# Kernel optimization log

Hardware: AMD Instinct MI355X
Metric: run time of the kernel (lower is better)

## Reference

```python
import jax, jax.numpy as jnp
import numpy as np

HW = 16          # feature map side before crop
P = HW * HW      # 256 spatial positions
G = 128          # output genetic channels per branch
CROP = 14        # crop size


def feature_genetic(x, idx, oh, ow):
    # x: [B, C, 16, 16]; idx: [G, P] channel index per (group, position);
    # oh, ow: [G] crop offsets in {0,1}
    B = x.shape[0]
    feat = x.reshape(B, x.shape[1], P)                 # [B, C, 256]
    pos = jnp.arange(P)
    picked = feat[:, idx, pos]                         # [B, G, 256]
    grid = picked.reshape(B, G, HW, HW)                # [B, 128, 16, 16]
    ch = jnp.arange(G)
    hidx = oh[:, None] + jnp.arange(CROP)[None, :]     # [G, 14]
    widx = ow[:, None] + jnp.arange(CROP)[None, :]     # [G, 14]
    # fancy-index crop: [B, 128, 14, 14]
    return grid[:, ch[:, None, None], hidx[:, :, None], widx[:, None, :]]


def setup_inputs() -> dict:
    key = jax.random.key(0)
    k1, k3, k5, kw, ki, kh, kw2 = jax.random.split(key, 7)
    B, C = 128, 512
    x1 = jax.random.normal(k1, (B, C, HW, HW), dtype=jnp.float32)
    x3 = jax.random.normal(k3, (B, C, HW, HW), dtype=jnp.float32)
    x5 = jax.random.normal(k5, (B, C, HW, HW), dtype=jnp.float32)
    W = jax.random.normal(kw, (768, 384), dtype=jnp.float32) * 0.02  # 1x1 conv weight
    idx = jax.random.randint(ki, (3, G, P), 0, C, dtype=jnp.int32)
    offh = jax.random.randint(kh, (3, G), 0, 2, dtype=jnp.int32)
    offw = jax.random.randint(kw2, (3, G), 0, 2, dtype=jnp.int32)
    return {"x1": x1, "x3": x3, "x5": x5, "W": W, "idx": idx, "offh": offh, "offw": offw}


def reference(x1, x3, x5, W, idx, offh, offw):
    g1 = feature_genetic(x1, idx[0], offh[0], offw[0])   # [B, 128, 14, 14]
    g3 = feature_genetic(x3, idx[1], offh[1], offw[1])
    g5 = feature_genetic(x5, idx[2], offh[2], offw[2])
    feats = jnp.concatenate((g1, g3, g5), axis=1)        # [B, 384, 14, 14]
    # 1x1 conv (no bias): Conv2d(384, 768, kernel_size=1)
    out = jnp.einsum('bchw,oc->bohw', feats, W)          # [B, 768, 14, 14]
    return out
```

## Files before the change

### kernel.cpp

```cpp
#include <hip/hip_runtime.h>
#include <hip/hip_bf16.h>

#define PIX 256
#define CROP 14
#define HW2 196
#define BB 128
#define CC 512
#define NC 384
#define NO 768
#define CAP 128

typedef __bf16 bf16x8 __attribute__((ext_vector_type(8)));
typedef __bf16 bf16x4 __attribute__((ext_vector_type(4)));
typedef float  f32x4  __attribute__((ext_vector_type(4)));
typedef unsigned int u32;

#define GLOAD_LDS16(src, dst) \
    __builtin_amdgcn_global_load_lds((const __attribute__((address_space(1))) void*)(src), \
                                     (__attribute__((address_space(3))) void*)(dst), 16, 0, 0)

__global__ void wconv_kernel(const float* __restrict__ W, __bf16* __restrict__ Wb) {
    int tid = blockIdx.x * 256 + threadIdx.x;
    Wb[tid] = (__bf16)W[tid];
}

__global__ void fill_kernel(const int* __restrict__ idx, const int* __restrict__ offh,
                            const int* __restrict__ offw, int* __restrict__ cnt,
                            u32* __restrict__ bucket) {
    int tid = blockIdx.x * 256 + threadIdx.x;
    int c3 = tid / HW2;
    int hw = tid - c3 * HW2;
    int i = hw / CROP, j = hw - i * CROP;
    int p = (offh[c3] + i) * 16 + offw[c3] + j;
    int ch = idx[c3 * PIX + p];
    int bkt = (c3 >> 7) * CC + ch;
    int pos = atomicAdd(&cnt[bkt], 1);
    if (pos < CAP) bucket[bkt * CAP + pos] = ((u32)c3 << 16) | ((u32)hw << 8) | (u32)p;
}

#define LSTR 260
__global__ __launch_bounds__(256) void scatter_kernel(
        const float* __restrict__ x1, const float* __restrict__ x3,
        const float* __restrict__ x5, const int* __restrict__ cnt,
        const u32* __restrict__ bucket, __bf16* __restrict__ fT) {
    __shared__ __bf16 lds[64 * LSTR];
    int bx = blockIdx.x;
    int E = cnt[bx]; if (E > CAP) E = CAP;
    if (E == 0) return;
    int b0 = blockIdx.y * 64;
    int t = bx >> 9, ch = bx & 511;
    const float* x = (t == 0) ? x1 : (t == 1) ? x3 : x5;
    int w = threadIdx.x >> 6, lane = threadIdx.x & 63;
    for (int r = w; r < 64; r += 4) {
        f32x4 v = *(const f32x4*)(x + ((size_t)(b0 + r) * CC + ch) * PIX + lane * 4);
        bf16x4 q;
        q[0] = (__bf16)v[0]; q[1] = (__bf16)v[1]; q[2] = (__bf16)v[2]; q[3] = (__bf16)v[3];
        *(bf16x4*)&lds[r * LSTR + lane * 4] = q;
    }
    __syncthreads();
    for (int e = w; e < E; e += 4) {
        u32 pk = bucket[bx * CAP + e];
        int c3 = pk >> 16, hw = (pk >> 8) & 255, p = pk & 255;
        fT[((size_t)c3 * HW2 + hw) * BB + b0 + lane] = lds[lane * LSTR + p];
    }
}

__global__ __launch_bounds__(256) void ftrans_kernel(const __bf16* __restrict__ fT,
                                                     __bf16* __restrict__ feats) {
    __shared__ __bf16 lds[64 * 128];
    int hw = blockIdx.x;
    int c0 = blockIdx.y * 64;
    int t = threadIdx.x;
    int l16 = t & 15;
#pragma unroll
    for (int r4 = 0; r4 < 4; ++r4) {
        int cr = (t >> 4) + r4 * 16;
        bf16x8 v = *(const bf16x8*)(fT + ((size_t)(c0 + cr) * HW2 + hw) * BB + l16 * 8);
        int chunk = l16 ^ ((cr >> 3) & 7);
        *(bf16x8*)&lds[cr * 128 + chunk * 8] = v;
    }
    __syncthreads();
    int cg = t & 7;
#pragma unroll
    for (int r = 0; r < 4; ++r) {
        int b = (t >> 3) + r * 32;
        bf16x8 ov;
#pragma unroll
        for (int k = 0; k < 8; ++k) {
            int c = cg * 8 + k;
            ov[k] = lds[c * 128 + (((b >> 3) ^ cg) * 8) + (b & 7)];
        }
        *(bf16x8*)(feats + ((size_t)b * HW2 + hw) * NC + c0 + cg * 8) = ov;
    }
}

__global__ __launch_bounds__(256) void gemm_kernel(const __bf16* __restrict__ feats,
                                                   const __bf16* __restrict__ Wb,
                                                   float* __restrict__ out) {
    __shared__ __bf16 ldsbuf[16384];
    __bf16* Abuf = ldsbuf;
    __bf16* Bbuf = ldsbuf + 8192;

    const int d = blockIdx.x;
    const int wg = (d & 7) * 147 + (d >> 3);
    const int o_base = (wg % 6) * 128;
    const int m_base = (wg / 6) * 128;

    const int tid = threadIdx.x;
    const int wave = tid >> 6, lane = tid & 63;
    const int wo = wave >> 1, wm = wave & 1;
    const int l15 = lane & 15, g = lane >> 4;
    const int xr = l15 & 7;

    f32x4 acc[4][4] = {};

    for (int kt = 0; kt < 6; ++kt) {
        const int k0g = kt * 64;
#pragma unroll
        for (int it = 0; it < 4; ++it) {
            int ck = tid + it * 256;
            int row = ck >> 3, cc = ck & 7;
            int koff = k0g + ((cc ^ (row & 7)) << 3);
            GLOAD_LDS16(Wb    + (size_t)(o_base + row) * NC + koff, Abuf + ck * 8);
            GLOAD_LDS16(feats + (size_t)(m_base + row) * NC + koff, Bbuf + ck * 8);
        }
        __syncthreads();
#pragma unroll
        for (int k0 = 0; k0 < 64; k0 += 32) {
            const int cb = (k0 >> 3) + g;
            bf16x8 a[4], b[4];
#pragma unroll
            for (int s = 0; s < 4; ++s) {
                int arow = wo * 64 + s * 16 + l15;
                a[s] = *(const bf16x8*)&Abuf[arow * 64 + ((cb ^ xr) << 3)];
                int brow = wm * 64 + s * 16 + l15;
                b[s] = *(const bf16x8*)&Bbuf[brow * 64 + ((cb ^ xr) << 3)];
            }
#pragma unroll
            for (int os = 0; os < 4; ++os)
#pragma unroll
                for (int ms = 0; ms < 4; ++ms)
                    acc[os][ms] = __builtin_amdgcn_mfma_f32_16x16x32_bf16(a[os], b[ms], acc[os][ms], 0, 0, 0);
        }
        __syncthreads();
    }

#pragma unroll
    for (int os = 0; os < 4; ++os)
#pragma unroll
        for (int ms = 0; ms < 4; ++ms) {
            int m = m_base + wm * 64 + ms * 16 + l15;
            int bb = m / HW2;
            int hw = m - bb * HW2;
            int o = o_base + wo * 64 + os * 16 + g * 4;
            float* dst = out + ((size_t)bb * NO + o) * HW2 + hw;
            f32x4 v = acc[os][ms];
            dst[0 * HW2] = v[0];
            dst[1 * HW2] = v[1];
            dst[2 * HW2] = v[2];
            dst[3 * HW2] = v[3];
        }
}

extern "C" void kernel_launch(void* const* d_in, const int* in_sizes, int n_in,
                              void* d_out, int out_size, void* d_ws, size_t ws_size,
                              hipStream_t stream) {
    const float* x1   = (const float*)d_in[0];
    const float* x3   = (const float*)d_in[1];
    const float* x5   = (const float*)d_in[2];
    const float* W    = (const float*)d_in[3];
    const int*   idx  = (const int*)d_in[4];
    const int*   offh = (const int*)d_in[5];
    const int*   offw = (const int*)d_in[6];
    float* out = (float*)d_out;

    char* ws = (char*)d_ws;
    __bf16* fT     = (__bf16*)(ws);
    __bf16* feats  = (__bf16*)(ws + 19267584);
    __bf16* Wb     = (__bf16*)(ws + 38535168);
    int*    cnt    = (int*)   (ws + 39124992);
    u32*    bucket = (u32*)   (ws + 39131136);

    wconv_kernel<<<(NO * NC) / 256, 256, 0, stream>>>(W, Wb);
    hipMemsetAsync(cnt, 0, 1536 * sizeof(int), stream);
    fill_kernel<<<(NC * HW2) / 256, 256, 0, stream>>>(idx, offh, offw, cnt, bucket);
    scatter_kernel<<<dim3(1536, 2), 256, 0, stream>>>(x1, x3, x5, cnt, bucket, fT);
    ftrans_kernel<<<dim3(HW2, 6), 256, 0, stream>>>(fT, feats);
    gemm_kernel<<<1176, 256, 0, stream>>>(feats, Wb, out);
}
```

Measured before the change: 110.3 us.

## Replace bucketed scatter plus transpose with per-batch gather into LDS

The per-channel bucket scatter, which wrote a channel-major intermediate, and the separate transpose kernel are replaced by a prefix scan and compaction of the bucket entries into one dense list per branch. A new per-(batch, branch) kernel gathers the selected elements directly from x into an LDS tile and writes feats rows coalesced. This removes the fT intermediate round trip and the transpose pass, but the gathers from x are now scattered 4-byte loads rather than whole-row vector loads. It also adds two small launches, one of them a single-block scan.

```diff
diff --git a/kernel.cpp b/kernel.cpp
--- a/kernel.cpp
+++ b/kernel.cpp
@@ -9,6 +9,7 @@
 #define NC 384
 #define NO 768
 #define CAP 128
+#define ENT_T 25088
 
 typedef __bf16 bf16x8 __attribute__((ext_vector_type(8)));
 typedef __bf16 bf16x4 __attribute__((ext_vector_type(4)));
@@ -35,62 +36,81 @@
     int ch = idx[c3 * PIX + p];
     int bkt = (c3 >> 7) * CC + ch;
     int pos = atomicAdd(&cnt[bkt], 1);
-    if (pos < CAP) bucket[bkt * CAP + pos] = ((u32)c3 << 16) | ((u32)hw << 8) | (u32)p;
-}
-
-#define LSTR 260
+    if (pos < CAP)
+        bucket[bkt * CAP + pos] =
+            ((u32)(c3 & 127) << 25) | ((u32)hw << 17) | ((u32)p << 9) | (u32)ch;
+}
+
+__global__ __launch_bounds__(256) void scan_kernel(const int* __restrict__ cnt,
+                                                   int* __restrict__ pref) {
+    __shared__ int part[256];
+    int tid = threadIdx.x;
+    int loc[6];
+    int s = 0;
+#pragma unroll
+    for (int i = 0; i < 6; ++i) {
+        int v = cnt[tid * 6 + i]; if (v > CAP) v = CAP;
+        loc[i] = s; s += v;
+    }
+    part[tid] = s;
+    __syncthreads();
+    if (tid < 64) {
+        int l4[4]; int s4 = 0;
+#pragma unroll
+        for (int i = 0; i < 4; ++i) { l4[i] = s4; s4 += part[tid * 4 + i]; }
+        int v = s4;
+#pragma unroll
+        for (int d = 1; d < 64; d <<= 1) { int u = __shfl_up(v, d); if (tid >= d) v += u; }
+        int excl = v - s4;
+#pragma unroll
+        for (int i = 0; i < 4; ++i) part[tid * 4 + i] = excl + l4[i];
+    }
+    __syncthreads();
+    int off = part[tid];
+#pragma unroll
+    for (int i = 0; i < 6; ++i) pref[tid * 6 + i] = off + loc[i];
+}
+
+__global__ __launch_bounds__(128) void compact_kernel(const int* __restrict__ cnt,
+                                                      const int* __restrict__ pref,
+                                                      const u32* __restrict__ bucket,
+                                                      u32* __restrict__ ent) {
+    int bkt = blockIdx.x;
+    int E = cnt[bkt]; if (E > CAP) E = CAP;
+    int tid = threadIdx.x;
+    if (tid < E) ent[pref[bkt] + tid] = bucket[bkt * CAP + tid];
+}
+
 __global__ __launch_bounds__(256) void scatter_kernel(
         const float* __restrict__ x1, const float* __restrict__ x3,
-        const float* __restrict__ x5, const int* __restrict__ cnt,
-        const u32* __restrict__ bucket, __bf16* __restrict__ fT) {
-    __shared__ __bf16 lds[64 * LSTR];
-    int bx = blockIdx.x;
-    int E = cnt[bx]; if (E > CAP) E = CAP;
-    if (E == 0) return;
-    int b0 = blockIdx.y * 64;
-    int t = bx >> 9, ch = bx & 511;
+        const float* __restrict__ x5, const u32* __restrict__ ent,
+        __bf16* __restrict__ feats) {
+    __shared__ __bf16 fl[HW2 * 128];
+    int blk = blockIdx.x;
+    int b = blk / 3;
+    int t = blk - b * 3;
     const float* x = (t == 0) ? x1 : (t == 1) ? x3 : x5;
-    int w = threadIdx.x >> 6, lane = threadIdx.x & 63;
-    for (int r = w; r < 64; r += 4) {
-        f32x4 v = *(const f32x4*)(x + ((size_t)(b0 + r) * CC + ch) * PIX + lane * 4);
-        bf16x4 q;
-        q[0] = (__bf16)v[0]; q[1] = (__bf16)v[1]; q[2] = (__bf16)v[2]; q[3] = (__bf16)v[3];
-        *(bf16x4*)&lds[r * LSTR + lane * 4] = q;
+    const float* xb = x + (size_t)b * CC * PIX;
+    const u32* el = ent + t * ENT_T;
+    int tid = threadIdx.x;
+
+#pragma unroll 4
+    for (int g = tid; g < ENT_T; g += 256) {
+        u32 wd = el[g];
+        int ch = wd & 511;
+        int p  = (wd >> 9) & 255;
+        int hw = (wd >> 17) & 255;
+        int c3 = wd >> 25;
+        float f = xb[ch * PIX + p];
+        fl[hw * 128 + c3] = (__bf16)f;
     }
     __syncthreads();
-    for (int e = w; e < E; e += 4) {
-        u32 pk = bucket[bx * CAP + e];
-        int c3 = pk >> 16, hw = (pk >> 8) & 255, p = pk & 255;
-        fT[((size_t)c3 * HW2 + hw) * BB + b0 + lane] = lds[lane * LSTR + p];
-    }
-}
-
-__global__ __launch_bounds__(256) void ftrans_kernel(const __bf16* __restrict__ fT,
-                                                     __bf16* __restrict__ feats) {
-    __shared__ __bf16 lds[64 * 128];
-    int hw = blockIdx.x;
-    int c0 = blockIdx.y * 64;
-    int t = threadIdx.x;
-    int l16 = t & 15;
-#pragma unroll
-    for (int r4 = 0; r4 < 4; ++r4) {
-        int cr = (t >> 4) + r4 * 16;
-        bf16x8 v = *(const bf16x8*)(fT + ((size_t)(c0 + cr) * HW2 + hw) * BB + l16 * 8);
-        int chunk = l16 ^ ((cr >> 3) & 7);
-        *(bf16x8*)&lds[cr * 128 + chunk * 8] = v;
-    }
-    __syncthreads();
-    int cg = t & 7;
-#pragma unroll
-    for (int r = 0; r < 4; ++r) {
-        int b = (t >> 3) + r * 32;
-        bf16x8 ov;
-#pragma unroll
-        for (int k = 0; k < 8; ++k) {
-            int c = cg * 8 + k;
-            ov[k] = lds[c * 128 + (((b >> 3) ^ cg) * 8) + (b & 7)];
-        }
-        *(bf16x8*)(feats + ((size_t)b * HW2 + hw) * NC + c0 + cg * 8) = ov;
+
+    const size_t obase = (size_t)b * HW2 * NC + (size_t)t * 128;
+#pragma unroll 4
+    for (int i2 = tid; i2 < HW2 * 32; i2 += 256) {
+        int hw = i2 >> 5, cq = (i2 & 31) * 4;
+        *(bf16x4*)(feats + obase + (size_t)hw * NC + cq) = *(const bf16x4*)&fl[hw * 128 + cq];
     }
 }
 
@@ -175,16 +195,18 @@
     float* out = (float*)d_out;
 
     char* ws = (char*)d_ws;
-    __bf16* fT     = (__bf16*)(ws);
-    __bf16* feats  = (__bf16*)(ws + 19267584);
-    __bf16* Wb     = (__bf16*)(ws + 38535168);
-    int*    cnt    = (int*)   (ws + 39124992);
-    u32*    bucket = (u32*)   (ws + 39131136);
+    __bf16* feats  = (__bf16*)(ws);
+    __bf16* Wb     = (__bf16*)(ws + 19267584);
+    int*    cnt    = (int*)   (ws + 19857408);
+    int*    pref   = (int*)   (ws + 19863552);
+    u32*    bucket = (u32*)   (ws + 19869696);
+    u32*    ent    = (u32*)   (ws + 20656128);
 
     wconv_kernel<<<(NO * NC) / 256, 256, 0, stream>>>(W, Wb);
     hipMemsetAsync(cnt, 0, 1536 * sizeof(int), stream);
     fill_kernel<<<(NC * HW2) / 256, 256, 0, stream>>>(idx, offh, offw, cnt, bucket);
-    scatter_kernel<<<dim3(1536, 2), 256, 0, stream>>>(x1, x3, x5, cnt, bucket, fT);
-    ftrans_kernel<<<dim3(HW2, 6), 256, 0, stream>>>(fT, feats);
+    scan_kernel<<<1, 256, 0, stream>>>(cnt, pref);
+    compact_kernel<<<1536, 128, 0, stream>>>(cnt, pref, bucket, ent);
+    scatter_kernel<<<384, 256, 0, stream>>>(x1, x3, x5, ent, feats);
     gemm_kernel<<<1176, 256, 0, stream>>>(feats, Wb, out);
 }
```

Result: faster. 107.7 us (-2.3%).
